# Optimization experiments

Hardware: AMD Instinct MI355X
Metric: run time of the kernel (lower is better)

## Reference

```python
import jax, jax.numpy as jnp
import numpy as np

B, T, IN, H, OUT = 256, 512, 8, 128, 3


def setup_inputs() -> dict:
    key = jax.random.key(0)
    ks = jax.random.split(key, 16)
    s = 1.0 / np.sqrt(H)  # PyTorch LSTM init bound

    def u(k, shape):
        return jax.random.uniform(k, shape, jnp.float32, -s, s)

    inp = {"x": jax.random.normal(ks[0], (B, T, IN), jnp.float32)}
    ins = [IN, H, H]
    i = 1
    for l in range(3):
        inp[f"Wih{l}"] = u(ks[i], (4 * H, ins[l]))
        inp[f"Whh{l}"] = u(ks[i + 1], (4 * H, H))
        inp[f"bih{l}"] = u(ks[i + 2], (4 * H,))
        inp[f"bhh{l}"] = u(ks[i + 3], (4 * H,))
        i += 4
    inp["Wfc"] = u(ks[13], (OUT, H))
    inp["bfc"] = u(ks[14], (OUT,))
    return inp


def _lstm_layer(x, Wih, Whh, bih, bhh):
    # x: [T, B, in] -> (all hidden states [T, B, H], final hidden [B, H])
    # Precompute input contribution for every timestep (one big GEMM).
    xg = jnp.einsum('tbi,gi->tbg', x, Wih) + (bih + bhh)  # [T, B, 4H]

    def step(carry, xg_t):
        h, c = carry
        gates = xg_t + h @ Whh.T  # [B, 4H]
        i_, f_, g_, o_ = jnp.split(gates, 4, axis=-1)  # PyTorch gate order i,f,g,o
        c = jax.nn.sigmoid(f_) * c + jax.nn.sigmoid(i_) * jnp.tanh(g_)
        h = jax.nn.sigmoid(o_) * jnp.tanh(c)
        return (h, c), h

    h0 = jnp.zeros((x.shape[1], Whh.shape[1]), x.dtype)
    (hT, _), hs = jax.lax.scan(step, (h0, h0), xg)
    return hs, hT


def reference(x, Wih0, Whh0, bih0, bhh0, Wih1, Whh1, bih1, bhh1,
              Wih2, Whh2, bih2, bhh2, Wfc, bfc):
    xt = jnp.swapaxes(x, 0, 1)  # [T, B, IN]
    h1, _ = _lstm_layer(xt, Wih0, Whh0, bih0, bhh0)
    h2, _ = _lstm_layer(h1, Wih1, Whh1, bih1, bhh1)
    _, hT = _lstm_layer(h2, Wih2, Whh2, bih2, bhh2)  # only last step needed
    return hT @ Wfc.T + bfc  # [B, OUT]
```

## Files before the change

kernel.cpp:

```cpp
#include <hip/hip_runtime.h>

#define Bsz 256
#define Tt  512
#define Hh  128

#define OFF_WTHH 196608
#define OFF_BIAS 393216
#define OFF_HBUF 394752
#define OFF_FLAG 1181184
#define FLAG_N   6144

#define SKG(k) ((((k) >> 3) * 12) + ((k) & 7))

typedef unsigned long long u64;
typedef unsigned int u32;

__device__ __forceinline__ void st_h_agent(u64* p, float v, u32 seq) {
    u64 u = ((u64)seq << 32) | (u64)__float_as_uint(v);
    __hip_atomic_store(p, u, __ATOMIC_RELAXED, __HIP_MEMORY_SCOPE_AGENT);
}
__device__ __forceinline__ u64 ld_u64_agent(const u64* p) {
    return __hip_atomic_load(p, __ATOMIC_RELAXED, __HIP_MEMORY_SCOPE_AGENT);
}

__device__ __forceinline__ float4 stage4(const u64* __restrict__ src, u32 exp) {
    u64 a, b, c, d;
    for (;;) {
        a = ld_u64_agent(src + 0);
        b = ld_u64_agent(src + 1);
        c = ld_u64_agent(src + 2);
        d = ld_u64_agent(src + 3);
        if ((u32)(a >> 32) == exp && (u32)(b >> 32) == exp &&
            (u32)(c >> 32) == exp && (u32)(d >> 32) == exp) break;
    }
    return make_float4(__uint_as_float((u32)a), __uint_as_float((u32)b),
                       __uint_as_float((u32)c), __uint_as_float((u32)d));
}

template<int N>
__device__ __forceinline__ float row_shr_add(float v) {
    int s = __builtin_amdgcn_update_dpp(0, __float_as_int(v), 0x110 + N, 0xF, 0xF, true);
    return v + __int_as_float(s);
}
__device__ __forceinline__ float4 red16(float4 s) {
    s.x = row_shr_add<1>(s.x); s.x = row_shr_add<2>(s.x); s.x = row_shr_add<4>(s.x); s.x = row_shr_add<8>(s.x);
    s.y = row_shr_add<1>(s.y); s.y = row_shr_add<2>(s.y); s.y = row_shr_add<4>(s.y); s.y = row_shr_add<8>(s.y);
    s.z = row_shr_add<1>(s.z); s.z = row_shr_add<2>(s.z); s.z = row_shr_add<4>(s.z); s.z = row_shr_add<8>(s.z);
    s.w = row_shr_add<1>(s.w); s.w = row_shr_add<2>(s.w); s.w = row_shr_add<4>(s.w); s.w = row_shr_add<8>(s.w);
    return s;
}

#define FMA4(S, A, W) { S.x = fmaf(A, W.x, S.x); S.y = fmaf(A, W.y, S.y); \
                        S.z = fmaf(A, W.z, S.z); S.w = fmaf(A, W.w, S.w); }

__global__ void prep_kernel(const float* Wih0, const float* Whh0, const float* bih0, const float* bhh0,
                            const float* Wih1, const float* Whh1, const float* bih1, const float* bhh1,
                            const float* Wih2, const float* Whh2, const float* bih2, const float* bhh2,
                            float* ws)
{
    int gid = blockIdx.x * blockDim.x + threadIdx.x;
    if (gid < FLAG_N) ((int*)(ws + OFF_FLAG))[gid] = -1;
    u64* hb = (u64*)(ws + OFF_HBUF);
    for (int i = gid; i < 4 * 3 * 256 * 128; i += 6144) hb[i] = 0xFFFFFFFF00000000ull;
    if (gid >= 3 * 512) return;
    int l = gid >> 9, gc = gid & 511;
    const float* Wih = (l == 0) ? Wih0 : (l == 1) ? Wih1 : Wih2;
    const float* Whh = (l == 0) ? Whh0 : (l == 1) ? Whh1 : Whh2;
    const float* bih = (l == 0) ? bih0 : (l == 1) ? bih1 : bih2;
    const float* bhh = (l == 0) ? bhh0 : (l == 1) ? bhh1 : bhh2;
    int Kin = (l == 0) ? 8 : 128;
    float* Wt_ih = ws + (size_t)l * 128 * 512;
    float* Wt_hh = ws + OFF_WTHH + (size_t)l * 128 * 512;
    float* bias  = ws + OFF_BIAS + l * 512;
    for (int k = 0; k < 128; k++) Wt_ih[k * 512 + gc] = (k < Kin) ? Wih[gc * Kin + k] : 0.f;
    for (int k = 0; k < 128; k++) Wt_hh[k * 512 + gc] = Whh[gc * 128 + k];
    bias[gc] = bih[gc] + bhh[gc];
}

__global__ __launch_bounds__(512, 2) void lstm_kernel(const float* __restrict__ x,
                                                      float* __restrict__ ws)
{
    const float* __restrict__ bias = ws + OFF_BIAS;
    u64* __restrict__ hbuf = (u64*)(ws + OFF_HBUF);
    int* __restrict__ fl = (int*)(ws + OFF_FLAG);

    const int layer = blockIdx.x >> 6;
    const int tile  = blockIdx.x & 63;
    const int rt  = tile & 15;
    const int hct = tile >> 4;
    const int r0  = rt << 4;
    const int hc0 = hct << 5;
    const int tid = threadIdx.x;

    __shared__ float sAin[16][192];
    __shared__ float sArec[16][192];
    __shared__ float sG[16][132];

    for (int i = tid; i < 16 * 192; i += 512) ((float*)sAin)[i] = 0.f;

    int* adflag = nullptr;
    if (tid < 4)                    adflag = fl + ((layer * 16 + rt) * 4 + tid) * 32;
    else if (tid < 8 && layer < 2)  adflag = fl + (((layer + 1) * 16 + rt) * 4 + (tid - 4)) * 32;
    int* myflag = fl + ((layer * 16 + rt) * 4 + hct) * 32;

    const int kg = tid & 15;
    const int rg = (tid >> 4) & 1;
    const int cg = tid >> 5;
    const int cbase = cg << 3;
    const int gcb = ((cbase >> 5) << 7) + hc0 + (cbase & 31);
    const int ka = kg * 12;

    const float* Wl_ih = ws + (size_t)layer * 65536;
    const float* Wl_hh = ws + OFF_WTHH + (size_t)layer * 65536;
    float4 wihA[8], wihB[8], whhA[8], whhB[8];
#pragma unroll
    for (int kk = 0; kk < 8; kk++) {
        int k = kg * 8 + kk;
        wihA[kk] = *(const float4*)&Wl_ih[(size_t)k * 512 + gcb];
        wihB[kk] = *(const float4*)&Wl_ih[(size_t)k * 512 + gcb + 4];
        whhA[kk] = *(const float4*)&Wl_hh[(size_t)k * 512 + gcb];
        whhB[kk] = *(const float4*)&Wl_hh[(size_t)k * 512 + gcb + 4];
    }
    float4 bias4a = *(const float4*)&bias[layer * 512 + gcb];
    float4 bias4b = *(const float4*)&bias[layer * 512 + gcb + 4];
    if (kg != 15) {
        bias4a = make_float4(0.f, 0.f, 0.f, 0.f);
        bias4b = make_float4(0.f, 0.f, 0.f, 0.f);
    }

    const int sr = tid >> 5;
    const int sk = (tid & 31) << 2;
    const int skc = SKG(sk);

    const int ur = tid >> 5, uc = tid & 31;
    float creg = 0.f;

    __syncthreads();

    for (int t = 0; t < Tt; ++t) {
        const int s = t + layer;
        const int prev = (s - 1) & 3, cur = s & 3;
        const u32 expseq = (u32)(s - 1);

        if (adflag != nullptr) {
            const int target = s - 3;
            while (__hip_atomic_load(adflag, __ATOMIC_RELAXED, __HIP_MEMORY_SCOPE_AGENT) < target)
                ;
        }

        if (layer == 0) {
            if (tid < 128) {
                int r = tid >> 3, i = tid & 7;
                sAin[r][i] = x[((size_t)(r0 + r) * Tt + t) * 8 + i];
            }
        } else {
            const u64* src = hbuf + ((size_t)prev * 3 + (layer - 1)) * Bsz * Hh
                           + (size_t)(r0 + sr) * Hh + sk;
            *(float4*)&sAin[sr][skc] = stage4(src, expseq);
        }
        if (t > 0) {
            const u64* src = hbuf + ((size_t)prev * 3 + layer) * Bsz * Hh
                           + (size_t)(r0 + sr) * Hh + sk;
            *(float4*)&sArec[sr][skc] = stage4(src, expseq);
        }
        __syncthreads();

        if (tid == 0)
            __hip_atomic_store(myflag, s, __ATOMIC_RELAXED, __HIP_MEMORY_SCOPE_AGENT);

#pragma unroll
        for (int j = 0; j < 8; j++) {
            const int r = rg * 8 + j;
            float4 acc0 = bias4a, acc1 = bias4b;
            {
                float4 a0 = *(const float4*)&sAin[r][ka];
                float4 a1 = *(const float4*)&sAin[r][ka + 4];
                FMA4(acc0, a0.x, wihA[0]); FMA4(acc1, a0.x, wihB[0]);
                FMA4(acc0, a0.y, wihA[1]); FMA4(acc1, a0.y, wihB[1]);
                FMA4(acc0, a0.z, wihA[2]); FMA4(acc1, a0.z, wihB[2]);
                FMA4(acc0, a0.w, wihA[3]); FMA4(acc1, a0.w, wihB[3]);
                FMA4(acc0, a1.x, wihA[4]); FMA4(acc1, a1.x, wihB[4]);
                FMA4(acc0, a1.y, wihA[5]); FMA4(acc1, a1.y, wihB[5]);
                FMA4(acc0, a1.z, wihA[6]); FMA4(acc1, a1.z, wihB[6]);
                FMA4(acc0, a1.w, wihA[7]); FMA4(acc1, a1.w, wihB[7]);
            }
            if (t > 0) {
                float4 b0 = *(const float4*)&sArec[r][ka];
                float4 b1 = *(const float4*)&sArec[r][ka + 4];
                FMA4(acc0, b0.x, whhA[0]); FMA4(acc1, b0.x, whhB[0]);
                FMA4(acc0, b0.y, whhA[1]); FMA4(acc1, b0.y, whhB[1]);
                FMA4(acc0, b0.z, whhA[2]); FMA4(acc1, b0.z, whhB[2]);
                FMA4(acc0, b0.w, whhA[3]); FMA4(acc1, b0.w, whhB[3]);
                FMA4(acc0, b1.x, whhA[4]); FMA4(acc1, b1.x, whhB[4]);
                FMA4(acc0, b1.y, whhA[5]); FMA4(acc1, b1.y, whhB[5]);
                FMA4(acc0, b1.z, whhA[6]); FMA4(acc1, b1.z, whhB[6]);
                FMA4(acc0, b1.w, whhA[7]); FMA4(acc1, b1.w, whhB[7]);
            }
            acc0 = red16(acc0);
            acc1 = red16(acc1);
            if (kg == 15) {
                *(float4*)&sG[r][cbase]     = acc0;
                *(float4*)&sG[r][cbase + 4] = acc1;
            }
        }
        __syncthreads();

        {
            float gi = sG[ur][uc],      gf = sG[ur][32 + uc];
            float gg = sG[ur][64 + uc], go = sG[ur][96 + uc];
            float si = 1.f / (1.f + __expf(-gi));
            float sf = 1.f / (1.f + __expf(-gf));
            float so = 1.f / (1.f + __expf(-go));
            creg = sf * creg + si * tanhf(gg);
            u64* dst = hbuf + ((size_t)cur * 3 + layer) * Bsz * Hh
                     + (size_t)(r0 + ur) * Hh + hc0 + uc;
            st_h_agent(dst, so * tanhf(creg), (u32)s);
        }
    }
}

__global__ void fc_kernel(const float* __restrict__ ws, const float* __restrict__ Wfc,
                          const float* __restrict__ bfc, float* __restrict__ out)
{
    const u64* h2 = (const u64*)(ws + OFF_HBUF) + (size_t)(1 * 3 + 2) * Bsz * Hh;
    int b = threadIdx.x;
    float a0 = bfc[0], a1 = bfc[1], a2 = bfc[2];
    for (int k = 0; k < 128; k++) {
        float h = __uint_as_float((u32)h2[b * 128 + k]);
        a0 += h * Wfc[0 * 128 + k];
        a1 += h * Wfc[1 * 128 + k];
        a2 += h * Wfc[2 * 128 + k];
    }
    out[b * 3 + 0] = a0;
    out[b * 3 + 1] = a1;
    out[b * 3 + 2] = a2;
}

extern "C" void kernel_launch(void* const* d_in, const int* in_sizes, int n_in,
                              void* d_out, int out_size, void* d_ws, size_t ws_size,
                              hipStream_t stream)
{
    const float* x = (const float*)d_in[0];
    float* ws = (float*)d_ws;

    prep_kernel<<<24, 256, 0, stream>>>(
        (const float*)d_in[1],  (const float*)d_in[2],  (const float*)d_in[3],  (const float*)d_in[4],
        (const float*)d_in[5],  (const float*)d_in[6],  (const float*)d_in[7],  (const float*)d_in[8],
        (const float*)d_in[9],  (const float*)d_in[10], (const float*)d_in[11], (const float*)d_in[12],
        ws);

    void* args[2] = { (void*)&x, (void*)&ws };
    hipLaunchCooperativeKernel((void*)lstm_kernel, dim3(192), dim3(512), args, 0, stream);

    fc_kernel<<<1, 256, 0, stream>>>(ws, (const float*)d_in[13], (const float*)d_in[14], (float*)d_out);
}
```

Measured before the change: 3.223 ms.

## Give each block full hidden width for 4 rows to keep recurrence local

Each block now owns 4 batch rows across all 128 hidden units and 512 gates, so the recurrent hidden state stays in shared memory. This removes the cross-block global polling for the layer's own previous step. Only the cross-layer handoff still goes through flagged global buffers, and the recurrent FMAs are issued before waiting on the input layer. Weights are streamed each step from a prepacked global layout instead of held in registers, and tanh uses an exp-based approximation. The trade is more weight traffic per step through L2/L1 in exchange for fewer synchronisation round-trips.

```diff
diff --git a/kernel.cpp b/kernel.cpp
--- a/kernel.cpp
+++ b/kernel.cpp
@@ -4,11 +4,10 @@
 #define Tt  512
 #define Hh  128
 
-#define OFF_WTHH 196608
 #define OFF_BIAS 393216
 #define OFF_HBUF 394752
 #define OFF_FLAG 1181184
-#define FLAG_N   6144
+#define FLAG_N   4096
 
 #define SKG(k) ((((k) >> 3) * 12) + ((k) & 7))
 
@@ -23,18 +22,13 @@
     return __hip_atomic_load(p, __ATOMIC_RELAXED, __HIP_MEMORY_SCOPE_AGENT);
 }
 
-__device__ __forceinline__ float4 stage4(const u64* __restrict__ src, u32 exp) {
-    u64 a, b, c, d;
-    for (;;) {
-        a = ld_u64_agent(src + 0);
-        b = ld_u64_agent(src + 1);
-        c = ld_u64_agent(src + 2);
-        d = ld_u64_agent(src + 3);
-        if ((u32)(a >> 32) == exp && (u32)(b >> 32) == exp &&
-            (u32)(c >> 32) == exp && (u32)(d >> 32) == exp) break;
-    }
-    return make_float4(__uint_as_float((u32)a), __uint_as_float((u32)b),
-                       __uint_as_float((u32)c), __uint_as_float((u32)d));
+__device__ __forceinline__ float fast_tanh(float x) {
+    float e = __expf(2.f * x);
+    return 1.f - 2.f / (e + 1.f);
+}
+
+__device__ __forceinline__ float f4c(const float4& v, int i) {
+    switch (i & 3) { case 0: return v.x; case 1: return v.y; case 2: return v.z; default: return v.w; }
 }
 
 template<int N>
@@ -61,20 +55,36 @@
     int gid = blockIdx.x * blockDim.x + threadIdx.x;
     if (gid < FLAG_N) ((int*)(ws + OFF_FLAG))[gid] = -1;
     u64* hb = (u64*)(ws + OFF_HBUF);
-    for (int i = gid; i < 4 * 3 * 256 * 128; i += 6144) hb[i] = 0xFFFFFFFF00000000ull;
-    if (gid >= 3 * 512) return;
-    int l = gid >> 9, gc = gid & 511;
+    for (int i = gid; i < 4 * 3 * 256 * 128; i += 98304) hb[i] = 0xFFFFFFFF00000000ull;
+
+    if (gid < 1536) {
+        int l = gid >> 9, gc = gid & 511;
+        const float* bih = (l == 0) ? bih0 : (l == 1) ? bih1 : bih2;
+        const float* bhh = (l == 0) ? bhh0 : (l == 1) ? bhh1 : bhh2;
+        ws[OFF_BIAS + l * 512 + gc] = bih[gc] + bhh[gc];
+    }
+
+    int l    = gid >> 15;
+    int r1   = gid & 32767;
+    int w    = r1 >> 12;
+    int r2   = r1 & 4095;
+    int j    = r2 >> 6;
+    int lane = r2 & 63;
+    int tid  = w * 64 + lane;
+    int kg   = tid & 15, og = tid >> 4;
     const float* Wih = (l == 0) ? Wih0 : (l == 1) ? Wih1 : Wih2;
     const float* Whh = (l == 0) ? Whh0 : (l == 1) ? Whh1 : Whh2;
-    const float* bih = (l == 0) ? bih0 : (l == 1) ? bih1 : bih2;
-    const float* bhh = (l == 0) ? bhh0 : (l == 1) ? bhh1 : bhh2;
     int Kin = (l == 0) ? 8 : 128;
-    float* Wt_ih = ws + (size_t)l * 128 * 512;
-    float* Wt_hh = ws + OFF_WTHH + (size_t)l * 128 * 512;
-    float* bias  = ws + OFF_BIAS + l * 512;
-    for (int k = 0; k < 128; k++) Wt_ih[k * 512 + gc] = (k < Kin) ? Wih[gc * Kin + k] : 0.f;
-    for (int k = 0; k < 128; k++) Wt_hh[k * 512 + gc] = Whh[gc * 128 + k];
-    bias[gc] = bih[gc] + bhh[gc];
+    float v[4];
+    for (int qq = 0; qq < 4; qq++) {
+        int jj = (j < 32) ? j : j - 32;
+        int q = jj * 4 + qq;
+        int k = kg * 8 + (q >> 4);
+        int c = og * 16 + (q & 15);
+        v[qq] = (j < 32) ? ((k < Kin) ? Wih[c * Kin + k] : 0.f)
+                         : Whh[c * 128 + k];
+    }
+    ((float4*)ws)[gid] = make_float4(v[0], v[1], v[2], v[3]);
 }
 
 __global__ __launch_bounds__(512, 2) void lstm_kernel(const float* __restrict__ x,
@@ -85,55 +95,39 @@
     int* __restrict__ fl = (int*)(ws + OFF_FLAG);
 
     const int layer = blockIdx.x >> 6;
-    const int tile  = blockIdx.x & 63;
-    const int rt  = tile & 15;
-    const int hct = tile >> 4;
-    const int r0  = rt << 4;
-    const int hc0 = hct << 5;
-    const int tid = threadIdx.x;
-
-    __shared__ float sAin[16][192];
-    __shared__ float sArec[16][192];
-    __shared__ float sG[16][132];
-
-    for (int i = tid; i < 16 * 192; i += 512) ((float*)sAin)[i] = 0.f;
-
-    int* adflag = nullptr;
-    if (tid < 4)                    adflag = fl + ((layer * 16 + rt) * 4 + tid) * 32;
-    else if (tid < 8 && layer < 2)  adflag = fl + (((layer + 1) * 16 + rt) * 4 + (tid - 4)) * 32;
-    int* myflag = fl + ((layer * 16 + rt) * 4 + hct) * 32;
-
-    const int kg = tid & 15;
-    const int rg = (tid >> 4) & 1;
-    const int cg = tid >> 5;
-    const int cbase = cg << 3;
-    const int gcb = ((cbase >> 5) << 7) + hc0 + (cbase & 31);
-    const int ka = kg * 12;
-
-    const float* Wl_ih = ws + (size_t)layer * 65536;
-    const float* Wl_hh = ws + OFF_WTHH + (size_t)layer * 65536;
-    float4 wihA[8], wihB[8], whhA[8], whhB[8];
-#pragma unroll
-    for (int kk = 0; kk < 8; kk++) {
-        int k = kg * 8 + kk;
-        wihA[kk] = *(const float4*)&Wl_ih[(size_t)k * 512 + gcb];
-        wihB[kk] = *(const float4*)&Wl_ih[(size_t)k * 512 + gcb + 4];
-        whhA[kk] = *(const float4*)&Wl_hh[(size_t)k * 512 + gcb];
-        whhB[kk] = *(const float4*)&Wl_hh[(size_t)k * 512 + gcb + 4];
-    }
-    float4 bias4a = *(const float4*)&bias[layer * 512 + gcb];
-    float4 bias4b = *(const float4*)&bias[layer * 512 + gcb + 4];
-    if (kg != 15) {
-        bias4a = make_float4(0.f, 0.f, 0.f, 0.f);
-        bias4b = make_float4(0.f, 0.f, 0.f, 0.f);
-    }
-
-    const int sr = tid >> 5;
-    const int sk = (tid & 31) << 2;
-    const int skc = SKG(sk);
-
-    const int ur = tid >> 5, uc = tid & 31;
+    const int rt    = blockIdx.x & 63;
+    const int r0    = rt << 2;
+    const int tid   = threadIdx.x;
+
+    __shared__ float sAin[4][192];
+    __shared__ float hrec[4][192];
+    __shared__ float sG[4][516];
+
+    for (int i = tid; i < 4 * 192; i += 512) ((float*)sAin)[i] = 0.f;
+
+    const int kg   = tid & 15;
+    const int og   = tid >> 4;
+    const int w    = tid >> 6;
+    const int lane = tid & 63;
+
+    const float4* __restrict__ wq =
+        (const float4*)ws + ((size_t)layer << 15) + ((size_t)w << 12) + lane;
+
+    float4 bias4[4];
+#pragma unroll
+    for (int cq = 0; cq < 4; cq++)
+        bias4[cq] = (kg == 15) ? *(const float4*)&bias[layer * 512 + og * 16 + cq * 4]
+                               : make_float4(0.f, 0.f, 0.f, 0.f);
+
+    const int sr = tid >> 7, shc = tid & 127;
+    const int s_lds = SKG(shc);
+
+    const int ur = tid >> 7, uc = tid & 127;
+    const int u_lds = SKG(uc);
     float creg = 0.f;
+
+    int* myflag  = (layer >= 1) ? fl + ((layer - 1) * 64 + rt) * 32 : nullptr;
+    int* depflag = (layer <= 1) ? fl + (layer * 64 + rt) * 32 : nullptr;
 
     __syncthreads();
 
@@ -142,80 +136,113 @@
         const int prev = (s - 1) & 3, cur = s & 3;
         const u32 expseq = (u32)(s - 1);
 
-        if (adflag != nullptr) {
-            const int target = s - 3;
-            while (__hip_atomic_load(adflag, __ATOMIC_RELAXED, __HIP_MEMORY_SCOPE_AGENT) < target)
-                ;
-        }
-
-        if (layer == 0) {
-            if (tid < 128) {
-                int r = tid >> 3, i = tid & 7;
-                sAin[r][i] = x[((size_t)(r0 + r) * Tt + t) * 8 + i];
-            }
-        } else {
-            const u64* src = hbuf + ((size_t)prev * 3 + (layer - 1)) * Bsz * Hh
-                           + (size_t)(r0 + sr) * Hh + sk;
-            *(float4*)&sAin[sr][skc] = stage4(src, expseq);
-        }
+        u64 hv = 0; float xv = 0.f;
+        const u64* src = nullptr;
+        if (layer > 0) {
+            src = hbuf + ((size_t)prev * 3 + (layer - 1)) * Bsz * Hh
+                + (size_t)(r0 + sr) * Hh + shc;
+            hv = ld_u64_agent(src);
+        } else if (tid < 32) {
+            int r = tid >> 3, i = tid & 7;
+            xv = x[((size_t)(r0 + r) * Tt + t) * 8 + i];
+        }
+
+        float4 acc[16];
+#pragma unroll
+        for (int r = 0; r < 4; r++)
+#pragma unroll
+            for (int cq = 0; cq < 4; cq++) acc[r * 4 + cq] = bias4[cq];
+
         if (t > 0) {
-            const u64* src = hbuf + ((size_t)prev * 3 + layer) * Bsz * Hh
-                           + (size_t)(r0 + sr) * Hh + sk;
-            *(float4*)&sArec[sr][skc] = stage4(src, expseq);
+            float4 aR[4][2];
+#pragma unroll
+            for (int r = 0; r < 4; r++) {
+                aR[r][0] = *(const float4*)&hrec[r][kg * 12];
+                aR[r][1] = *(const float4*)&hrec[r][kg * 12 + 4];
+            }
+#pragma unroll
+            for (int kk = 0; kk < 8; kk++) {
+                float4 w0 = wq[(size_t)(32 + kk * 4 + 0) * 64];
+                float4 w1 = wq[(size_t)(32 + kk * 4 + 1) * 64];
+                float4 w2 = wq[(size_t)(32 + kk * 4 + 2) * 64];
+                float4 w3 = wq[(size_t)(32 + kk * 4 + 3) * 64];
+#pragma unroll
+                for (int r = 0; r < 4; r++) {
+                    float a = f4c(aR[r][kk >> 2], kk);
+                    FMA4(acc[r * 4 + 0], a, w0); FMA4(acc[r * 4 + 1], a, w1);
+                    FMA4(acc[r * 4 + 2], a, w2); FMA4(acc[r * 4 + 3], a, w3);
+                }
+            }
+        }
+
+        if (layer > 0) {
+            while ((u32)(hv >> 32) != expseq) hv = ld_u64_agent(src);
+            sAin[sr][s_lds] = __uint_as_float((u32)hv);
+        } else if (tid < 32) {
+            int r = tid >> 3, i = tid & 7;
+            sAin[r][i] = xv;
         }
         __syncthreads();
 
-        if (tid == 0)
-            __hip_atomic_store(myflag, s, __ATOMIC_RELAXED, __HIP_MEMORY_SCOPE_AGENT);
-
-#pragma unroll
-        for (int j = 0; j < 8; j++) {
-            const int r = rg * 8 + j;
-            float4 acc0 = bias4a, acc1 = bias4b;
-            {
-                float4 a0 = *(const float4*)&sAin[r][ka];
-                float4 a1 = *(const float4*)&sAin[r][ka + 4];
-                FMA4(acc0, a0.x, wihA[0]); FMA4(acc1, a0.x, wihB[0]);
-                FMA4(acc0, a0.y, wihA[1]); FMA4(acc1, a0.y, wihB[1]);
-                FMA4(acc0, a0.z, wihA[2]); FMA4(acc1, a0.z, wihB[2]);
-                FMA4(acc0, a0.w, wihA[3]); FMA4(acc1, a0.w, wihB[3]);
-                FMA4(acc0, a1.x, wihA[4]); FMA4(acc1, a1.x, wihB[4]);
-                FMA4(acc0, a1.y, wihA[5]); FMA4(acc1, a1.y, wihB[5]);
-                FMA4(acc0, a1.z, wihA[6]); FMA4(acc1, a1.z, wihB[6]);
-                FMA4(acc0, a1.w, wihA[7]); FMA4(acc1, a1.w, wihB[7]);
-            }
-            if (t > 0) {
-                float4 b0 = *(const float4*)&sArec[r][ka];
-                float4 b1 = *(const float4*)&sArec[r][ka + 4];
-                FMA4(acc0, b0.x, whhA[0]); FMA4(acc1, b0.x, whhB[0]);
-                FMA4(acc0, b0.y, whhA[1]); FMA4(acc1, b0.y, whhB[1]);
-                FMA4(acc0, b0.z, whhA[2]); FMA4(acc1, b0.z, whhB[2]);
-                FMA4(acc0, b0.w, whhA[3]); FMA4(acc1, b0.w, whhB[3]);
-                FMA4(acc0, b1.x, whhA[4]); FMA4(acc1, b1.x, whhB[4]);
-                FMA4(acc0, b1.y, whhA[5]); FMA4(acc1, b1.y, whhB[5]);
-                FMA4(acc0, b1.z, whhA[6]); FMA4(acc1, b1.z, whhB[6]);
-                FMA4(acc0, b1.w, whhA[7]); FMA4(acc1, b1.w, whhB[7]);
-            }
-            acc0 = red16(acc0);
-            acc1 = red16(acc1);
-            if (kg == 15) {
-                *(float4*)&sG[r][cbase]     = acc0;
-                *(float4*)&sG[r][cbase + 4] = acc1;
-            }
+        if (tid == 0) {
+            if (myflag != nullptr)
+                __hip_atomic_store(myflag, s, __ATOMIC_RELAXED, __HIP_MEMORY_SCOPE_AGENT);
+            if (depflag != nullptr) {
+                const int target = s - 3;
+                while (__hip_atomic_load(depflag, __ATOMIC_RELAXED, __HIP_MEMORY_SCOPE_AGENT) < target)
+                    __builtin_amdgcn_s_sleep(1);
+            }
+        }
+
+        {
+            float4 aR[4][2];
+#pragma unroll
+            for (int r = 0; r < 4; r++) {
+                aR[r][0] = *(const float4*)&sAin[r][kg * 12];
+                aR[r][1] = *(const float4*)&sAin[r][kg * 12 + 4];
+            }
+#pragma unroll
+            for (int kk = 0; kk < 8; kk++) {
+                float4 w0 = wq[(size_t)(kk * 4 + 0) * 64];
+                float4 w1 = wq[(size_t)(kk * 4 + 1) * 64];
+                float4 w2 = wq[(size_t)(kk * 4 + 2) * 64];
+                float4 w3 = wq[(size_t)(kk * 4 + 3) * 64];
+#pragma unroll
+                for (int r = 0; r < 4; r++) {
+                    float a = f4c(aR[r][kk >> 2], kk);
+                    FMA4(acc[r * 4 + 0], a, w0); FMA4(acc[r * 4 + 1], a, w1);
+                    FMA4(acc[r * 4 + 2], a, w2); FMA4(acc[r * 4 + 3], a, w3);
+                }
+            }
+        }
+
+#pragma unroll
+        for (int i = 0; i < 16; i++) acc[i] = red16(acc[i]);
+        if (kg == 15) {
+#pragma unroll
+            for (int r = 0; r < 4; r++)
+#pragma unroll
+                for (int cq = 0; cq < 4; cq++)
+                    *(float4*)&sG[r][og * 16 + cq * 4] = acc[r * 4 + cq];
         }
         __syncthreads();
 
         {
-            float gi = sG[ur][uc],      gf = sG[ur][32 + uc];
-            float gg = sG[ur][64 + uc], go = sG[ur][96 + uc];
+            float gi = sG[ur][uc],        gf = sG[ur][128 + uc];
+            float gg = sG[ur][256 + uc],  go = sG[ur][384 + uc];
             float si = 1.f / (1.f + __expf(-gi));
             float sf = 1.f / (1.f + __expf(-gf));
             float so = 1.f / (1.f + __expf(-go));
-            creg = sf * creg + si * tanhf(gg);
-            u64* dst = hbuf + ((size_t)cur * 3 + layer) * Bsz * Hh
-                     + (size_t)(r0 + ur) * Hh + hc0 + uc;
-            st_h_agent(dst, so * tanhf(creg), (u32)s);
-        }
+            creg = sf * creg + si * fast_tanh(gg);
+            float h = so * fast_tanh(creg);
+            hrec[ur][u_lds] = h;
+            if (layer < 2 || t == Tt - 1) {
+                u64* dst = hbuf + ((size_t)cur * 3 + layer) * Bsz * Hh
+                         + (size_t)(r0 + ur) * Hh + uc;
+                st_h_agent(dst, h, (u32)s);
+            }
+        }
+        __syncthreads();
     }
 }
 
@@ -243,7 +270,7 @@
     const float* x = (const float*)d_in[0];
     float* ws = (float*)d_ws;
 
-    prep_kernel<<<24, 256, 0, stream>>>(
+    prep_kernel<<<384, 256, 0, stream>>>(
         (const float*)d_in[1],  (const float*)d_in[2],  (const float*)d_in[3],  (const float*)d_in[4],
         (const float*)d_in[5],  (const float*)d_in[6],  (const float*)d_in[7],  (const float*)d_in[8],
         (const float*)d_in[9],  (const float*)d_in[10], (const float*)d_in[11], (const float*)d_in[12],
```

New measurement: 9.389 ms. 191% more time.
